# Kernel optimization log

Hardware: AMD Instinct MI355X
Metric: run time of the kernel (lower is better)

Reference implementation:

```python
import jax, jax.numpy as jnp
import numpy as np

STEPLIM = 20   # module steplim; loop runs while iter <= steplim -> steplim+1 iterations
TOL = 1e-4     # early-stopping tolerance on change in mean NN error


def _nn1(pc1, pc2):
    """1-NN of each point in pc1 [B,N,3] within pc2 [B,M,3] under L2 norm.
    Uses the GEMM form ||a||^2 + ||b||^2 - 2 a.b instead of materializing the
    [B,N,M,3] broadcasted difference tensor. Returns (min_dist [B,N], idx [B,N])."""
    d2 = (jnp.sum(pc1 * pc1, axis=-1)[..., :, None]
          + jnp.sum(pc2 * pc2, axis=-1)[..., None, :]
          - 2.0 * jnp.einsum('bnd,bmd->bnm', pc1, pc2))
    d2 = jnp.maximum(d2, 1e-12)                  # clamp FP cancellation negatives
    idx = jnp.argmin(d2, axis=-1)                # [B, N]
    dmin = jnp.sqrt(jnp.take_along_axis(d2, idx[..., None], axis=-1)[..., 0])
    return dmin, idx


def _kabsch(src, dst):
    """Rigid transform (R, t) minimizing ||R@src + t - dst|| via SVD (EPnP._points_transform)."""
    c1 = jnp.mean(src, axis=-2, keepdims=True)   # [B,1,3]
    c2 = jnp.mean(dst, axis=-2, keepdims=True)
    H = jnp.einsum('bni,bnj->bij', src - c1, dst - c2)          # [B,3,3]
    U, S, Vt = jnp.linalg.svd(H, full_matrices=False)
    det = jnp.linalg.det(jnp.einsum('bki,bjk->bij', Vt, U))     # det(V U^T)
    d = jnp.sign(det)
    D = jnp.stack([jnp.ones_like(d), jnp.ones_like(d), d], axis=-1)  # reflection fix
    R = jnp.einsum('bki,bk,bjk->bij', Vt, D, U)                 # V diag(1,1,d) U^T
    t = c2[..., 0, :] - jnp.einsum('bij,bj->bi', R, c1[..., 0, :])
    return R, t


def _icp(p1, p2):
    B = p1.shape[0]

    def step(carry, _):
        pc, err, done = carry
        dmin, idx = _nn1(pc, p2)
        # errnew = sum(sum(values)/len(values)): mean over batch of per-point sums
        errnew = jnp.sum(dmin) / B
        # source quirk: uses the LAST batch element's indices for all batches
        matched = p2[:, idx[-1], :]                              # [B,N,3]
        R, t = _kabsch(pc, matched)
        pc_new = jnp.einsum('bij,bnj->bni', R, pc) + t[:, None, :]
        # torch loop updates temppc BEFORE the break check, then freezes
        pc_out = jnp.where(done, pc, pc_new)
        err_out = jnp.where(done, err, errnew)
        done_out = done | (jnp.abs(err - errnew) < TOL)
        return (pc_out, err_out, done_out), None

    init = (p1, jnp.asarray(0.0, p1.dtype), jnp.asarray(False))
    (pc, _, _), _ = jax.lax.scan(step, init, None, length=STEPLIM + 1)
    R, t = _kabsch(p1, pc)
    return jnp.concatenate([R, t[..., None]], axis=-1)           # [B,3,4] = [R | t]


def setup_inputs() -> dict:
    key = jax.random.key(0)
    k1, k2 = jax.random.split(key)
    p1 = jax.random.normal(k1, (1, 8192, 3), dtype=jnp.float32)
    p2 = jax.random.normal(k2, (1, 8192, 3), dtype=jnp.float32)
    return {"p1": p1, "p2": p2}


def reference(p1, p2):
    return _icp(p1, p2)
```

## Files before the change

kernel.cpp:

```cpp
#include <hip/hip_runtime.h>
#include <math.h>

#define N_PTS 8192
#define ICP_STEPS 21
#define ICP_TOL 1e-4

#define NBLK 256
#define BSIZE 512
#define QPW 4
#define CH 4096
#define NCH 2
#define NSETS 16

struct IcpCtl {
  double err;
  double Rc[9];
  double tc[3];
  int done;
};

__global__ __launch_bounds__(256) void icp_prep(const float* __restrict__ p2,
                                                float4* __restrict__ p2aug,
                                                IcpCtl* __restrict__ ctl,
                                                double* __restrict__ acc,
                                                unsigned* __restrict__ gtick,
                                                unsigned* __restrict__ root) {
  int t = blockIdx.x * 256 + threadIdx.x;
  float x = p2[3*t], y = p2[3*t+1], z = p2[3*t+2];
  p2aug[t] = make_float4(x, y, z, fmaf(x, x, fmaf(y, y, z*z)));
  if (t < NSETS * 16) acc[t] = 0.0;
  if (t < NSETS) gtick[t << 4] = 0u;
  if (t == 0) {
    *root = 0u;
    ctl->err = 0.0; ctl->done = 0;
    #pragma unroll
    for (int i = 0; i < 9; ++i) ctl->Rc[i] = (i % 4 == 0) ? 1.0 : 0.0;
    ctl->tc[0] = ctl->tc[1] = ctl->tc[2] = 0.0;
  }
}

__device__ __forceinline__ void kabsch_solve(const double* s, double* R, double* T) {
  const double n = (double)N_PTS;
  const double c1x = s[1]/n, c1y = s[2]/n, c1z = s[3]/n;
  const double c2x = s[4]/n, c2y = s[5]/n, c2z = s[6]/n;
  const double h00 = s[7]  - n*c1x*c2x, h01 = s[8]  - n*c1x*c2y, h02 = s[9]  - n*c1x*c2z;
  const double h10 = s[10] - n*c1y*c2x, h11 = s[11] - n*c1y*c2y, h12 = s[12] - n*c1y*c2z;
  const double h20 = s[13] - n*c1z*c2x, h21 = s[14] - n*c1z*c2y, h22 = s[15] - n*c1z*c2z;

  double a00 = h00*h00 + h10*h10 + h20*h20;
  double a01 = h00*h01 + h10*h11 + h20*h21;
  double a02 = h00*h02 + h10*h12 + h20*h22;
  double a11 = h01*h01 + h11*h11 + h21*h21;
  double a12 = h01*h02 + h11*h12 + h21*h22;
  double a22 = h02*h02 + h12*h12 + h22*h22;

  double v00=1.0, v01=0.0, v02=0.0;
  double v10=0.0, v11=1.0, v12=0.0;
  double v20=0.0, v21=0.0, v22=1.0;

#define ROT3(app, aqq, apq, arp, arq, vpa, vqa, vpb, vqb, vpc, vqc)              \
  {                                                                              \
    double apq_ = apq;                                                           \
    if (fabs(apq_) > 1e-300) {                                                   \
      double tau = (aqq - app) / (2.0 * apq_);                                   \
      double tt  = (tau >= 0.0 ? 1.0 : -1.0) / (fabs(tau) + sqrt(1.0 + tau*tau));\
      double c_  = 1.0 / sqrt(1.0 + tt*tt), sn = tt * c_;                        \
      app -= tt * apq_;  aqq += tt * apq_;  apq = 0.0;                           \
      double t1 = arp, t2 = arq;                                                 \
      arp = c_*t1 - sn*t2;  arq = sn*t1 + c_*t2;                                 \
      t1 = vpa; t2 = vqa; vpa = c_*t1 - sn*t2; vqa = sn*t1 + c_*t2;              \
      t1 = vpb; t2 = vqb; vpb = c_*t1 - sn*t2; vqb = sn*t1 + c_*t2;              \
      t1 = vpc; t2 = vqc; vpc = c_*t1 - sn*t2; vqc = sn*t1 + c_*t2;              \
    }                                                                            \
  }

  #pragma unroll
  for (int sweep = 0; sweep < 6; ++sweep) {
    ROT3(a00, a11, a01, a02, a12, v00, v01, v10, v11, v20, v21);
    ROT3(a00, a22, a02, a01, a12, v00, v02, v10, v12, v20, v22);
    ROT3(a11, a22, a12, a01, a02, v01, v02, v11, v12, v21, v22);
  }
#undef ROT3

  double l0 = a00, l1 = a11, l2 = a22;
  double e0x=v00, e0y=v10, e0z=v20;
  double e1x=v01, e1y=v11, e1z=v21;
  double e2x=v02, e2y=v12, e2z=v22;
#define CSWAP(la, lb, xa, ya, za, xb, yb, zb)                                    \
  if (lb > la) { double t_;                                                      \
    t_ = la; la = lb; lb = t_;  t_ = xa; xa = xb; xb = t_;                       \
    t_ = ya; ya = yb; yb = t_;  t_ = za; za = zb; zb = t_; }
  CSWAP(l0, l1, e0x, e0y, e0z, e1x, e1y, e1z);
  CSWAP(l0, l2, e0x, e0y, e0z, e2x, e2y, e2z);
  CSWAP(l1, l2, e1x, e1y, e1z, e2x, e2y, e2z);
#undef CSWAP

  double detV = e0x*(e1y*e2z - e1z*e2y) - e0y*(e1x*e2z - e1z*e2x)
              + e0z*(e1x*e2y - e1y*e2x);
  const double dsg = (detV >= 0.0) ? 1.0 : -1.0;

  double u0x = h00*e0x + h01*e0y + h02*e0z;
  double u0y = h10*e0x + h11*e0y + h12*e0z;
  double u0z = h20*e0x + h21*e0y + h22*e0z;
  double n0 = sqrt(u0x*u0x + u0y*u0y + u0z*u0z);
  if (!(n0 > 1e-150)) {
    R[0]=1.0; R[1]=0.0; R[2]=0.0; R[3]=0.0; R[4]=1.0; R[5]=0.0;
    R[6]=0.0; R[7]=0.0; R[8]=1.0;
    T[0]=c2x-c1x; T[1]=c2y-c1y; T[2]=c2z-c1z;
    return;
  }
  u0x /= n0; u0y /= n0; u0z /= n0;
  double u1x = h00*e1x + h01*e1y + h02*e1z;
  double u1y = h10*e1x + h11*e1y + h12*e1z;
  double u1z = h20*e1x + h21*e1y + h22*e1z;
  const double d10 = u1x*u0x + u1y*u0y + u1z*u0z;
  u1x -= d10*u0x; u1y -= d10*u0y; u1z -= d10*u0z;
  double n1 = sqrt(u1x*u1x + u1y*u1y + u1z*u1z);
  if (!(n1 > 1e-150)) {
    R[0]=1.0; R[1]=0.0; R[2]=0.0; R[3]=0.0; R[4]=1.0; R[5]=0.0;
    R[6]=0.0; R[7]=0.0; R[8]=1.0;
    T[0]=c2x-c1x; T[1]=c2y-c1y; T[2]=c2z-c1z;
    return;
  }
  u1x /= n1; u1y /= n1; u1z /= n1;
  const double u2x = u0y*u1z - u0z*u1y;
  const double u2y = u0z*u1x - u0x*u1z;
  const double u2z = u0x*u1y - u0y*u1x;

  R[0] = e0x*u0x + e1x*u1x + dsg*e2x*u2x;
  R[1] = e0x*u0y + e1x*u1y + dsg*e2x*u2y;
  R[2] = e0x*u0z + e1x*u1z + dsg*e2x*u2z;
  R[3] = e0y*u0x + e1y*u1x + dsg*e2y*u2x;
  R[4] = e0y*u0y + e1y*u1y + dsg*e2y*u2y;
  R[5] = e0y*u0z + e1y*u1z + dsg*e2y*u2z;
  R[6] = e0z*u0x + e1z*u1x + dsg*e2z*u2x;
  R[7] = e0z*u0y + e1z*u1y + dsg*e2z*u2y;
  R[8] = e0z*u0z + e1z*u1z + dsg*e2z*u2z;
  T[0] = c2x - (R[0]*c1x + R[1]*c1y + R[2]*c1z);
  T[1] = c2y - (R[3]*c1x + R[4]*c1y + R[5]*c1z);
  T[2] = c2z - (R[6]*c1x + R[7]*c1y + R[8]*c1z);
}

__global__ __launch_bounds__(BSIZE) void icp_step(const float* __restrict__ p1,
                                                  const float4* __restrict__ p2aug,
                                                  IcpCtl* __restrict__ ctl,
                                                  double* __restrict__ acc,
                                                  unsigned* __restrict__ gtick,
                                                  unsigned* __restrict__ root,
                                                  float* __restrict__ out) {
  if (ctl->done) return;
  __shared__ float4 cand[CH];
  __shared__ unsigned long long pkbuf[8][5];
  __shared__ float4 qlds[32];
  __shared__ double pairbuf[32][17];
  __shared__ double setbuf[16][17];
  __shared__ double totbuf[16];
  __shared__ int solverFlag;

  const int tid  = threadIdx.x;
  const int lane = tid & 63;
  const int w    = tid >> 6;
  const int bid  = blockIdx.x;

  if (tid == 0) solverFlag = 0;

  const double R0 = ctl->Rc[0], R1 = ctl->Rc[1], R2 = ctl->Rc[2];
  const double R3 = ctl->Rc[3], R4 = ctl->Rc[4], R5 = ctl->Rc[5];
  const double R6 = ctl->Rc[6], R7 = ctl->Rc[7], R8 = ctl->Rc[8];
  const double T0 = ctl->tc[0], T1 = ctl->tc[1], T2 = ctl->tc[2];

  const int qb = (bid << 5) + (w << 2);
  float axv[QPW], ayv[QPW], azv[QPW], best[QPW];
  int bidx[QPW];
  #pragma unroll
  for (int j = 0; j < QPW; ++j) {
    const int q = qb + j;
    const double X = (double)p1[3*q], Y = (double)p1[3*q+1], Z = (double)p1[3*q+2];
    const float qx = (float)(R0*X + R1*Y + R2*Z + T0);
    const float qy = (float)(R3*X + R4*Y + R5*Z + T1);
    const float qz = (float)(R6*X + R7*Y + R8*Z + T2);
    axv[j] = -2.f*qx; ayv[j] = -2.f*qy; azv[j] = -2.f*qz;
    best[j] = __builtin_inff(); bidx[j] = 0;
    if (lane == 0) qlds[(w << 2) + j] = make_float4(qx, qy, qz, 0.f);
  }

  for (int cb = 0; cb < NCH; ++cb) {
    const int cbase = cb << 12;
    #pragma unroll
    for (int kk = 0; kk < 8; ++kk)
      cand[(kk << 9) + tid] = p2aug[cbase + (kk << 9) + tid];
    __syncthreads();
    #pragma unroll 4
    for (int kk = 0; kk < 64; ++kk) {
      const int cidx = cbase + (kk << 6) + lane;
      float4 c = cand[(kk << 6) + lane];
      #pragma unroll
      for (int j = 0; j < QPW; ++j) {
        float d = fmaf(axv[j], c.x, fmaf(ayv[j], c.y, fmaf(azv[j], c.z, c.w)));
        if (d < best[j]) { best[j] = d; bidx[j] = cidx; }
      }
    }
    __syncthreads();
  }

  unsigned long long pk[QPW];
  #pragma unroll
  for (int j = 0; j < QPW; ++j) {
    unsigned u = __float_as_uint(best[j]);
    u ^= (unsigned)((int)u >> 31) | 0x80000000u;
    pk[j] = ((unsigned long long)u << 32) | (unsigned)bidx[j];
  }
  #pragma unroll
  for (int j = 0; j < QPW; ++j) {
    #pragma unroll
    for (int o = 1; o < 64; o <<= 1) {
      unsigned long long other = __shfl_xor(pk[j], o, 64);
      pk[j] = (other < pk[j]) ? other : pk[j];
    }
  }
  if (lane == 0) {
    #pragma unroll
    for (int j = 0; j < QPW; ++j) pkbuf[w][j] = pk[j];
  }
  __syncthreads();

  if (tid < 32) {
    const unsigned long long m = pkbuf[tid >> 2][tid & 3];
    const unsigned idx = (unsigned)(m & 0xffffffffull);
    const float4 q4 = qlds[tid];
    const float4 b4 = p2aug[idx];
    const double ax = q4.x, ay = q4.y, az = q4.z;
    const double bx = b4.x, by = b4.y, bz = b4.z;
    const double d2 = (ax*ax + ay*ay + az*az) + (bx*bx + by*by + bz*bz)
                    - 2.0*(ax*bx + ay*by + az*bz);
    pairbuf[tid][0]  = sqrt(fmax(d2, 1e-12));
    pairbuf[tid][1]  = ax;    pairbuf[tid][2]  = ay;    pairbuf[tid][3]  = az;
    pairbuf[tid][4]  = bx;    pairbuf[tid][5]  = by;    pairbuf[tid][6]  = bz;
    pairbuf[tid][7]  = ax*bx; pairbuf[tid][8]  = ax*by; pairbuf[tid][9]  = ax*bz;
    pairbuf[tid][10] = ay*bx; pairbuf[tid][11] = ay*by; pairbuf[tid][12] = ay*bz;
    pairbuf[tid][13] = az*bx; pairbuf[tid][14] = az*by; pairbuf[tid][15] = az*bz;
  }
  __syncthreads();

  if (tid < 16) {
    double ssum = 0.0;
    #pragma unroll
    for (int i = 0; i < 32; ++i) ssum += pairbuf[i][tid];
    atomicAdd(acc + ((bid & 15) << 4) + tid, ssum);
  }
  if (tid == 0) {
    asm volatile("s_waitcnt vmcnt(0)" ::: "memory");
    const int gi = bid & 15;
    unsigned og = atomicAdd(gtick + (gi << 4), 1u);
    if (og == 15u) {
      unsigned orr = atomicAdd(root, 1u);
      if (orr == 15u) solverFlag = 1;
    }
  }
  __syncthreads();
  if (!solverFlag) return;

  double val = 0.0;
  if (tid < 256) val = atomicAdd(acc + tid, 0.0);
  if (tid < 256) setbuf[tid >> 4][tid & 15] = val;
  __syncthreads();
  if (tid < 16) {
    double t2 = 0.0;
    #pragma unroll
    for (int i = 0; i < 16; ++i) t2 += setbuf[i][tid];
    totbuf[tid] = t2;
  }
  __syncthreads();

  if (tid == 0) {
    double sm[16];
    #pragma unroll
    for (int i = 0; i < 16; ++i) sm[i] = totbuf[i];
    double R[9], T[3];
    kabsch_solve(sm, R, T);
    double Rc[9] = {R0,R1,R2,R3,R4,R5,R6,R7,R8};
    double tc[3] = {T0,T1,T2};
    double Rn[9], tn[3];
    #pragma unroll
    for (int i = 0; i < 3; ++i) {
      #pragma unroll
      for (int j = 0; j < 3; ++j)
        Rn[3*i+j] = R[3*i+0]*Rc[0+j] + R[3*i+1]*Rc[3+j] + R[3*i+2]*Rc[6+j];
      tn[i] = R[3*i+0]*tc[0] + R[3*i+1]*tc[1] + R[3*i+2]*tc[2] + T[i];
    }
    #pragma unroll
    for (int i = 0; i < 9; ++i) ctl->Rc[i] = Rn[i];
    #pragma unroll
    for (int i = 0; i < 3; ++i) ctl->tc[i] = tn[i];
    const double errnew = sm[0];
    ctl->done = (fabs(ctl->err - errnew) < ICP_TOL) ? 1 : 0;
    ctl->err  = errnew;
    #pragma unroll
    for (int i = 0; i < 3; ++i) {
      out[4*i + 0] = (float)Rn[3*i + 0];
      out[4*i + 1] = (float)Rn[3*i + 1];
      out[4*i + 2] = (float)Rn[3*i + 2];
      out[4*i + 3] = (float)tn[i];
    }
    *root = 0u;
  }
  if (tid < 256) acc[tid] = 0.0;
  if (tid < 16) gtick[tid << 4] = 0u;
}

extern "C" void kernel_launch(void* const* d_in, const int* in_sizes, int n_in,
                              void* d_out, int out_size, void* d_ws, size_t ws_size,
                              hipStream_t stream) {
  const float* p1 = (const float*)d_in[0];
  const float* p2 = (const float*)d_in[1];
  float* out = (float*)d_out;

  char* ws = (char*)d_ws;
  float4* p2aug  = (float4*)ws;
  IcpCtl* ctl    = (IcpCtl*)(ws + 128*1024);
  double* acc    = (double*)(ws + 132*1024);
  unsigned* gtick = (unsigned*)(ws + 136*1024);
  unsigned* root  = (unsigned*)(ws + 140*1024);

  icp_prep<<<N_PTS/256, 256, 0, stream>>>(p2, p2aug, ctl, acc, gtick, root);
  for (int it = 0; it < ICP_STEPS; ++it)
    icp_step<<<NBLK, BSIZE, 0, stream>>>(p1, p2aug, ctl, acc, gtick, root, out);
}
```

Before: 478.3 us.

## Split queries unevenly across block tiers with templated queries-per-wave

Replaces the uniform 4 queries per wave with four tiers of 64 blocks handling 6, 5, 3 and 2 queries per wave, covering all 8192 points. The aim is to balance work against the expected CU assignment, since the 256 blocks exceed 256 CUs only in some configurations, and to let the first-launched blocks carry more work. This adds template code size and divergent register pressure per tier, and the 6-query variant may raise VGPR use.

```diff
diff --git a/kernel.cpp b/kernel.cpp
--- a/kernel.cpp
+++ b/kernel.cpp
@@ -7,7 +7,6 @@
 
 #define NBLK 256
 #define BSIZE 512
-#define QPW 4
 #define CH 4096
 #define NCH 2
 #define NSETS 16
@@ -141,39 +140,30 @@
   T[2] = c2z - (R[6]*c1x + R[7]*c1y + R[8]*c1z);
 }
 
-__global__ __launch_bounds__(BSIZE) void icp_step(const float* __restrict__ p1,
-                                                  const float4* __restrict__ p2aug,
-                                                  IcpCtl* __restrict__ ctl,
-                                                  double* __restrict__ acc,
-                                                  unsigned* __restrict__ gtick,
-                                                  unsigned* __restrict__ root,
-                                                  float* __restrict__ out) {
-  if (ctl->done) return;
-  __shared__ float4 cand[CH];
-  __shared__ unsigned long long pkbuf[8][5];
-  __shared__ float4 qlds[32];
-  __shared__ double pairbuf[32][17];
-  __shared__ double setbuf[16][17];
-  __shared__ double totbuf[16];
-  __shared__ int solverFlag;
-
+template<int QW>
+__device__ __forceinline__ void icp_body(
+    const float* __restrict__ p1, const float4* __restrict__ p2aug,
+    IcpCtl* __restrict__ ctl, double* __restrict__ acc,
+    unsigned* __restrict__ gtick, unsigned* __restrict__ root,
+    float* __restrict__ out,
+    float4* cand, unsigned long long (*pkbuf)[7], float4* qlds,
+    double (*pairbuf)[17], double (*setbuf)[17], double* totbuf,
+    int* solverFlag, const int qbBlock) {
   const int tid  = threadIdx.x;
   const int lane = tid & 63;
   const int w    = tid >> 6;
   const int bid  = blockIdx.x;
 
-  if (tid == 0) solverFlag = 0;
-
   const double R0 = ctl->Rc[0], R1 = ctl->Rc[1], R2 = ctl->Rc[2];
   const double R3 = ctl->Rc[3], R4 = ctl->Rc[4], R5 = ctl->Rc[5];
   const double R6 = ctl->Rc[6], R7 = ctl->Rc[7], R8 = ctl->Rc[8];
   const double T0 = ctl->tc[0], T1 = ctl->tc[1], T2 = ctl->tc[2];
 
-  const int qb = (bid << 5) + (w << 2);
-  float axv[QPW], ayv[QPW], azv[QPW], best[QPW];
-  int bidx[QPW];
+  const int qb = qbBlock + w * QW;
+  float axv[QW], ayv[QW], azv[QW], best[QW];
+  int bidx[QW];
   #pragma unroll
-  for (int j = 0; j < QPW; ++j) {
+  for (int j = 0; j < QW; ++j) {
     const int q = qb + j;
     const double X = (double)p1[3*q], Y = (double)p1[3*q+1], Z = (double)p1[3*q+2];
     const float qx = (float)(R0*X + R1*Y + R2*Z + T0);
@@ -181,7 +171,7 @@
     const float qz = (float)(R6*X + R7*Y + R8*Z + T2);
     axv[j] = -2.f*qx; ayv[j] = -2.f*qy; azv[j] = -2.f*qz;
     best[j] = __builtin_inff(); bidx[j] = 0;
-    if (lane == 0) qlds[(w << 2) + j] = make_float4(qx, qy, qz, 0.f);
+    if (lane == 0) qlds[w * QW + j] = make_float4(qx, qy, qz, 0.f);
   }
 
   for (int cb = 0; cb < NCH; ++cb) {
@@ -195,7 +185,7 @@
       const int cidx = cbase + (kk << 6) + lane;
       float4 c = cand[(kk << 6) + lane];
       #pragma unroll
-      for (int j = 0; j < QPW; ++j) {
+      for (int j = 0; j < QW; ++j) {
         float d = fmaf(axv[j], c.x, fmaf(ayv[j], c.y, fmaf(azv[j], c.z, c.w)));
         if (d < best[j]) { best[j] = d; bidx[j] = cidx; }
       }
@@ -203,15 +193,15 @@
     __syncthreads();
   }
 
-  unsigned long long pk[QPW];
+  unsigned long long pk[QW];
   #pragma unroll
-  for (int j = 0; j < QPW; ++j) {
+  for (int j = 0; j < QW; ++j) {
     unsigned u = __float_as_uint(best[j]);
     u ^= (unsigned)((int)u >> 31) | 0x80000000u;
     pk[j] = ((unsigned long long)u << 32) | (unsigned)bidx[j];
   }
   #pragma unroll
-  for (int j = 0; j < QPW; ++j) {
+  for (int j = 0; j < QW; ++j) {
     #pragma unroll
     for (int o = 1; o < 64; o <<= 1) {
       unsigned long long other = __shfl_xor(pk[j], o, 64);
@@ -220,12 +210,12 @@
   }
   if (lane == 0) {
     #pragma unroll
-    for (int j = 0; j < QPW; ++j) pkbuf[w][j] = pk[j];
-  }
-  __syncthreads();
-
-  if (tid < 32) {
-    const unsigned long long m = pkbuf[tid >> 2][tid & 3];
+    for (int j = 0; j < QW; ++j) pkbuf[w][j] = pk[j];
+  }
+  __syncthreads();
+
+  if (tid < 8 * QW) {
+    const unsigned long long m = pkbuf[tid / QW][tid % QW];
     const unsigned idx = (unsigned)(m & 0xffffffffull);
     const float4 q4 = qlds[tid];
     const float4 b4 = p2aug[idx];
@@ -245,7 +235,7 @@
   if (tid < 16) {
     double ssum = 0.0;
     #pragma unroll
-    for (int i = 0; i < 32; ++i) ssum += pairbuf[i][tid];
+    for (int i = 0; i < 8 * QW; ++i) ssum += pairbuf[i][tid];
     atomicAdd(acc + ((bid & 15) << 4) + tid, ssum);
   }
   if (tid == 0) {
@@ -254,11 +244,11 @@
     unsigned og = atomicAdd(gtick + (gi << 4), 1u);
     if (og == 15u) {
       unsigned orr = atomicAdd(root, 1u);
-      if (orr == 15u) solverFlag = 1;
-    }
-  }
-  __syncthreads();
-  if (!solverFlag) return;
+      if (orr == 15u) *solverFlag = 1;
+    }
+  }
+  __syncthreads();
+  if (!*solverFlag) return;
 
   double val = 0.0;
   if (tid < 256) val = atomicAdd(acc + tid, 0.0);
@@ -308,6 +298,44 @@
   if (tid < 16) gtick[tid << 4] = 0u;
 }
 
+__global__ __launch_bounds__(BSIZE) void icp_step(const float* __restrict__ p1,
+                                                  const float4* __restrict__ p2aug,
+                                                  IcpCtl* __restrict__ ctl,
+                                                  double* __restrict__ acc,
+                                                  unsigned* __restrict__ gtick,
+                                                  unsigned* __restrict__ root,
+                                                  float* __restrict__ out) {
+  if (ctl->done) return;
+  __shared__ float4 cand[CH];
+  __shared__ unsigned long long pkbuf[8][7];
+  __shared__ float4 qlds[48];
+  __shared__ double pairbuf[48][17];
+  __shared__ double setbuf[16][17];
+  __shared__ double totbuf[16];
+  __shared__ int solverFlag;
+
+  if (threadIdx.x == 0) solverFlag = 0;
+
+  const int bid  = blockIdx.x;
+  const int tier = bid >> 6;
+  const int lb   = bid & 63;
+
+  switch (tier) {
+    case 0: icp_body<6>(p1, p2aug, ctl, acc, gtick, root, out, cand, pkbuf,
+                        qlds, pairbuf, setbuf, totbuf, &solverFlag,
+                        0    + lb * 48); break;
+    case 1: icp_body<5>(p1, p2aug, ctl, acc, gtick, root, out, cand, pkbuf,
+                        qlds, pairbuf, setbuf, totbuf, &solverFlag,
+                        3072 + lb * 40); break;
+    case 2: icp_body<3>(p1, p2aug, ctl, acc, gtick, root, out, cand, pkbuf,
+                        qlds, pairbuf, setbuf, totbuf, &solverFlag,
+                        5632 + lb * 24); break;
+    default: icp_body<2>(p1, p2aug, ctl, acc, gtick, root, out, cand, pkbuf,
+                        qlds, pairbuf, setbuf, totbuf, &solverFlag,
+                        7168 + lb * 16); break;
+  }
+}
+
 extern "C" void kernel_launch(void* const* d_in, const int* in_sizes, int n_in,
                               void* d_out, int out_size, void* d_ws, size_t ws_size,
                               hipStream_t stream) {
```

Measured after the change: 567.0 us. 1.19x slower.
